# Optimization experiments

Hardware: AMD Instinct MI355X
Metric: run time of the kernel (lower is better)

## Reference

```python
import jax, jax.numpy as jnp
import numpy as np

SQRT3 = float(np.sqrt(3.0))
TWO_PI = float(2.0 * np.pi)


def _safe_sqrt(x):
    return jnp.sqrt(jnp.clip(x, 1e-5))


def _matern(Q):
    # Matern 3/2 on the (already halved) quadratic form, matching torch matern()
    t = SQRT3 * _safe_sqrt(Q)
    return (1.0 + t) * jnp.exp(-t)


def _pairwise_kernel(x1, kp1, x2, kp2, scale):
    """Fused prob_product_quad + prob_product_constant + matern.

    x: [B,N,2] coords; kp: [B,N,3] = (e00, e11, e01) of SPD 2x2 E per point.
    Returns K [B,N,M].
    """
    a1, b1, c1 = kp1[..., 0], kp1[..., 1], kp1[..., 2]  # e00, e11, e01
    a2, b2, c2 = kp2[..., 0], kp2[..., 1], kp2[..., 2]
    det1 = a1 * b1 - c1 * c1  # det2x2(E1) [B,N]
    det2 = a2 * b2 - c2 * c2  # [B,M]
    s00 = a1[:, :, None] + a2[:, None, :]  # E1_00 + E2_00  [B,N,M]
    s11 = b1[:, :, None] + b2[:, None, :]
    s01 = c1[:, :, None] + c2[:, None, :]
    sdet = s00 * s11 - s01 * s01  # det(E1+E2)
    d = x1[:, :, None, :] - x2[:, None, :, :]  # [B,N,M,2]
    d0, d1 = d[..., 0], d[..., 1]
    Q = (s11 * d0 * d0 - 2.0 * s01 * d0 * d1 + s00 * d1 * d1) / sdet * 0.5
    C = 2.0 * (det1 ** 0.25)[:, :, None] * (det2 ** 0.25)[:, None, :] / _safe_sqrt(sdet)
    return _matern(Q) * C * scale


def _diag_kernel(kp, scale):
    # diagonal_prob_product: Q = 0, C = 2*sqrt(det E)/safe_sqrt(det(2E))
    a, b, c = kp[..., 0], kp[..., 1], kp[..., 2]
    det = a * b - c * c
    det2E = 4.0 * det  # det(2E) for 2x2
    C = 2.0 * jnp.sqrt(det) / _safe_sqrt(det2E)
    Q = jnp.zeros_like(C)
    return C * _matern(Q) * scale  # [B,N]


def setup_inputs() -> dict:
    key = jax.random.key(0)
    ks = jax.random.split(key, 8)
    B, N, M = 2, 1024, 16384

    def kparams(k, n):
        u = jax.random.uniform(k, (B, n, 3), dtype=jnp.float32)
        a = 0.5 + u[..., 0]
        b = 0.5 + u[..., 1]
        c = 0.2 * (u[..., 2] - 0.5)  # |c| small -> SPD
        return jnp.stack([a, b, c], axis=-1)

    coords_train = jax.random.uniform(ks[0], (B, N, 2), dtype=jnp.float32) * 512.0 / 64.0
    coords_test = jax.random.uniform(ks[1], (B, M, 2), dtype=jnp.float32) * 512.0 / 64.0
    kernel_params_train = kparams(ks[2], N)
    kernel_params_test = kparams(ks[3], M)
    y_train = jax.random.uniform(ks[4], (B, N, 1), dtype=jnp.float32) * 10.0
    var = 0.01 + 0.1 * jax.random.uniform(ks[5], (B, N), dtype=jnp.float32)
    mean = jnp.zeros((B, 1, 1), dtype=jnp.float32)
    scale_param = jnp.zeros((1,), dtype=jnp.float32)
    return {
        "coords_train": coords_train,
        "kernel_params_train": kernel_params_train,
        "coords_test": coords_test,
        "kernel_params_test": kernel_params_test,
        "y_train": y_train,
        "var": var,
        "mean": mean,
        "scale_param": scale_param,
    }


def reference(coords_train, kernel_params_train, coords_test, kernel_params_test,
              y_train, var, mean, scale_param):
    scale_prior = 1.0
    scale = scale_prior * jnp.exp(scale_param[0])  # CovarianceModule.get_scale
    B, N = coords_train.shape[0], coords_train.shape[1]

    # CovarianceModule / CrossCovarianceModule / DiagonalCovarianceModule
    K_nn = _pairwise_kernel(coords_train, kernel_params_train,
                            coords_train, kernel_params_train, scale)  # [B,N,N]
    K_nm = _pairwise_kernel(coords_train, kernel_params_train,
                            coords_test, kernel_params_test, scale)    # [B,N,M]
    K_mm_diag = _diag_kernel(kernel_params_test, scale)                 # [B,M]

    # GpSparseModule: A = K_nn + diag(var); chol; alpha = A^{-1}(y-mean); NLML
    eye = jnp.eye(N, dtype=K_nn.dtype)
    A = K_nn + var[..., None] * eye
    L = jnp.linalg.cholesky(A)
    y_centered = y_train - mean
    alpha = jax.scipy.linalg.cho_solve((L, True), y_centered)  # [B,N,1]
    data_fit = jnp.sum(y_centered * alpha, axis=1)             # [B,1]
    data_term = 0.5 * jnp.sum(data_fit, axis=1)                # [B]
    complexity_term = jnp.sum(jnp.log(jnp.diagonal(L, axis1=-2, axis2=-1)), axis=1)
    constant_term = 0.5 * N * np.log(TWO_PI)
    nlml = data_term + complexity_term + constant_term

    # GpDenseModule: predictive mean/variance at test points
    pred_mean = mean + jnp.einsum('bnm,bnk->bmk', K_nm, alpha)  # [B,M,1]
    v = jax.scipy.linalg.cho_solve((L, True), K_nm)             # [B,N,M]
    pred_var = (K_mm_diag - jnp.sum(K_nm * v, axis=1))[..., None]  # [B,M,1]
    return pred_mean, pred_var, nlml
```

## Files before the change

### kernel.cpp

```cpp
#include <hip/hip_runtime.h>
#include <math.h>

namespace {
constexpr int kB = 2;
constexpr int kN = 1024;
constexpr int kM = 16384;
constexpr float kSqrt3 = 1.7320508075688772f;

constexpr size_t A_BYTES = (size_t)kB * kN * kN * 4;
constexpr size_t DG_BYTES = (size_t)kB * 8 * 128 * 128 * 4;
constexpr size_t Z_BYTES = (size_t)kB * kN * 4;
constexpr size_t LH_BYTES = (size_t)kB * kN * kN * 2;
constexpr size_t DH_BYTES = (size_t)kB * 8 * 128 * 128 * 2;
constexpr size_t A_OFF = 0;
constexpr size_t DG_OFF = A_OFF + A_BYTES;
constexpr size_t Z_OFF = DG_OFF + DG_BYTES;
constexpr size_t LH_OFF = Z_OFF + Z_BYTES;
constexpr size_t LL_OFF = LH_OFF + LH_BYTES;
constexpr size_t DH_OFF = LL_OFF + LH_BYTES;
constexpr size_t DL_OFF = DH_OFF + DH_BYTES;
constexpr size_t WS_BYTES = DL_OFF + DH_BYTES;
}

typedef __attribute__((ext_vector_type(8))) short short8v;
typedef __attribute__((ext_vector_type(4))) float floatx4;

__device__ __forceinline__ float b16f(unsigned short h) {
  return __uint_as_float(((unsigned)h) << 16);
}
__device__ __forceinline__ void split_bf16(float x, unsigned short& h, unsigned short& l) {
  unsigned u = __float_as_uint(x);
  h = (unsigned short)(u >> 16);
  float rem = x - b16f(h);
  l = (unsigned short)(__float_as_uint(rem) >> 16);
}
__device__ __forceinline__ void pack2(float v0, float v1, unsigned& hw, unsigned& lw) {
  unsigned u0 = __float_as_uint(v0), u1 = __float_as_uint(v1);
  unsigned h0 = u0 & 0xFFFF0000u;
  unsigned h1 = u1 & 0xFFFF0000u;
  hw = (h0 >> 16) | h1;
  float r0 = v0 - __uint_as_float(h0);
  float r1 = v1 - __uint_as_float(h1);
  lw = (__float_as_uint(r0) >> 16) | (__float_as_uint(r1) & 0xFFFF0000u);
}

__device__ __forceinline__ float pair_kernel(
    float x0, float x1, float a1, float b1, float c1,
    float y0, float y1, float a2, float b2, float c2, float scale) {
  float det1 = a1 * b1 - c1 * c1;
  float det2 = a2 * b2 - c2 * c2;
  float s00 = a1 + a2, s11 = b1 + b2, s01 = c1 + c2;
  float sdet = s00 * s11 - s01 * s01;
  float d0 = x0 - y0, d1 = x1 - y1;
  float quad = s11 * d0 * d0 - 2.0f * s01 * d0 * d1 + s00 * d1 * d1;
  float Q = __fdividef(0.5f * quad, sdet);
  float x3 = 3.0f * fmaxf(Q, 1e-5f);
  float t = x3 * rsqrtf(x3);
  float C = 2.0f * sqrtf(sqrtf(det1)) * sqrtf(sqrtf(det2)) * rsqrtf(fmaxf(sdet, 1e-5f));
  return (1.0f + t) * __expf(-t) * C * scale;
}

__global__ __launch_bounds__(256) void build_A(
    const float* __restrict__ xt, const float* __restrict__ pt,
    const float* __restrict__ var, const float* __restrict__ sp,
    float* __restrict__ A) {
  int idx = blockIdx.x * 256 + threadIdx.x;
  int b = idx / (kN * kN);
  int r = (idx / kN) % kN;
  int c = idx % kN;
  float scale = __expf(sp[0]);
  const float* x1 = xt + ((size_t)b * kN + r) * 2;
  const float* p1 = pt + ((size_t)b * kN + r) * 3;
  const float* x2 = xt + ((size_t)b * kN + c) * 2;
  const float* p2 = pt + ((size_t)b * kN + c) * 3;
  float k = pair_kernel(x1[0], x1[1], p1[0], p1[1], p1[2],
                        x2[0], x2[1], p2[0], p2[1], p2[2], scale);
  if (r == c) k += var[b * kN + r];
  A[(size_t)idx] = k;
}

__device__ __forceinline__ void tri_decode(int idx, int& ti, int& tj) {
  float f = sqrtf(8.0f * (float)idx + 1.0f);
  int t0 = (int)((f - 1.0f) * 0.5f);
  while (t0 * (t0 + 1) / 2 > idx) --t0;
  while ((t0 + 1) * (t0 + 2) / 2 <= idx) ++t0;
  ti = t0;
  tj = idx - t0 * (t0 + 1) / 2;
}

__global__ __launch_bounds__(1024, 1) void chol_panel(float* __restrict__ A,
                                                      float* __restrict__ Dg,
                                                      unsigned short* __restrict__ Dh,
                                                      unsigned short* __restrict__ Dl, int p) {
  __shared__ float At[128 * 132];
  __shared__ float Dt[128 * 132];
  __shared__ float Tt[3 * 32 * 33];
  int b = blockIdx.x, t = threadIdx.x;
  float* Ab = A + (size_t)b * kN * kN;
  int r0 = p * 128;
#pragma unroll
  for (int q = 0; q < 4; ++q) {
    int idx = t + 1024 * q;
    int r = idx >> 5, c4 = idx & 31;
    *(float4*)&At[r * 132 + c4 * 4] = *(const float4*)&Ab[(size_t)(r0 + r) * kN + r0 + c4 * 4];
  }
  __syncthreads();
  int wave = t >> 6, lane = t & 63;
  int row0 = lane, row1 = lane + 64;
  for (int kb = 0; kb < 16; ++kb) {
    int K0 = kb * 8;
    int Kp = K0 - 8;
    if (kb > 0) {
      if (wave == 0) {
        int rr = lane >> 3, cc = lane & 7;
        float s = 0.0f;
#pragma unroll
        for (int e = 0; e < 8; ++e)
          s += At[(K0 + rr) * 132 + Kp + e] * At[(K0 + cc) * 132 + Kp + e];
        At[(K0 + rr) * 132 + K0 + cc] -= s;
      } else {
        int n = 120 - 8 * kb;
        int nt = n >> 2;
        int ntt = nt * (nt + 1) / 2;
        int base = K0 + 8;
        for (int idx = t - 64; idx < ntt; idx += 960) {
          int ti, tj;
          tri_decode(idx, ti, tj);
          int i0 = base + ti * 4, j0 = base + tj * 4;
          float Li[4][8], Lj[4][8];
#pragma unroll
          for (int r = 0; r < 4; ++r) {
            *(float4*)&Li[r][0] = *(const float4*)&At[(i0 + r) * 132 + Kp];
            *(float4*)&Li[r][4] = *(const float4*)&At[(i0 + r) * 132 + Kp + 4];
            *(float4*)&Lj[r][0] = *(const float4*)&At[(j0 + r) * 132 + Kp];
            *(float4*)&Lj[r][4] = *(const float4*)&At[(j0 + r) * 132 + Kp + 4];
          }
#pragma unroll
          for (int r = 0; r < 4; ++r) {
            float4 cv = *(const float4*)&At[(i0 + r) * 132 + j0];
            float cc4[4] = {cv.x, cv.y, cv.z, cv.w};
#pragma unroll
            for (int c = 0; c < 4; ++c) {
              float s = 0.0f;
#pragma unroll
              for (int e = 0; e < 8; ++e) s += Li[r][e] * Lj[c][e];
              cc4[c] -= s;
            }
            float4 ov = {cc4[0], cc4[1], cc4[2], cc4[3]};
            *(float4*)&At[(i0 + r) * 132 + j0] = ov;
          }
        }
      }
    }
    __syncthreads();
    if (wave == 0) {
      float rA0[8], rA1[8];
      *(float4*)&rA0[0] = *(const float4*)&At[row0 * 132 + K0];
      *(float4*)&rA0[4] = *(const float4*)&At[row0 * 132 + K0 + 4];
      *(float4*)&rA1[0] = *(const float4*)&At[row1 * 132 + K0];
      *(float4*)&rA1[4] = *(const float4*)&At[row1 * 132 + K0 + 4];
      if (kb > 0) {
        float pA0[8], pA1[8];
        *(float4*)&pA0[0] = *(const float4*)&At[row0 * 132 + Kp];
        *(float4*)&pA0[4] = *(const float4*)&At[row0 * 132 + Kp + 4];
        *(float4*)&pA1[0] = *(const float4*)&At[row1 * 132 + Kp];
        *(float4*)&pA1[4] = *(const float4*)&At[row1 * 132 + Kp + 4];
#pragma unroll
        for (int j = 0; j < 8; ++j) {
          float s0 = 0.0f, s1 = 0.0f;
#pragma unroll
          for (int e = 0; e < 8; ++e) {
            float pj = At[(K0 + j) * 132 + Kp + e];
            s0 += pA0[e] * pj;
            s1 += pA1[e] * pj;
          }
          rA0[j] -= s0;
          rA1[j] -= s1;
        }
      }
      float L11[8][8], idg[8];
#pragma unroll
      for (int r = 0; r < 8; ++r) {
        *(float4*)&L11[r][0] = *(const float4*)&At[(K0 + r) * 132 + K0];
        *(float4*)&L11[r][4] = *(const float4*)&At[(K0 + r) * 132 + K0 + 4];
      }
#pragma unroll
      for (int c = 0; c < 8; ++c) {
        float d = sqrtf(L11[c][c]);
        float iv = 1.0f / d;
        idg[c] = iv;
        L11[c][c] = d;
#pragma unroll
        for (int i = c + 1; i < 8; ++i) L11[i][c] *= iv;
#pragma unroll
        for (int j = c + 1; j < 8; ++j)
#pragma unroll
          for (int i = j; i < 8; ++i) L11[i][j] -= L11[i][c] * L11[j][c];
      }
      if (row0 >= K0 + 8) {
#pragma unroll
        for (int c = 0; c < 8; ++c) {
          float s = rA0[c];
#pragma unroll
          for (int j = 0; j < c; ++j) s -= rA0[j] * L11[c][j];
          rA0[c] = s * idg[c];
        }
      } else if (row0 >= K0) {
#pragma unroll
        for (int rr = 0; rr < 8; ++rr)
          if (row0 - K0 == rr) {
#pragma unroll
            for (int e = 0; e < 8; ++e) rA0[e] = (e <= rr) ? L11[rr][e] : 0.0f;
          }
      }
      if (row1 >= K0 + 8) {
#pragma unroll
        for (int c = 0; c < 8; ++c) {
          float s = rA1[c];
#pragma unroll
          for (int j = 0; j < c; ++j) s -= rA1[j] * L11[c][j];
          rA1[c] = s * idg[c];
        }
      } else if (row1 >= K0) {
#pragma unroll
        for (int rr = 0; rr < 8; ++rr)
          if (row1 - K0 == rr) {
#pragma unroll
            for (int e = 0; e < 8; ++e) rA1[e] = (e <= rr) ? L11[rr][e] : 0.0f;
          }
      }
      if (row0 >= K0) {
        float4 v0 = {rA0[0], rA0[1], rA0[2], rA0[3]};
        float4 v1 = {rA0[4], rA0[5], rA0[6], rA0[7]};
        *(float4*)&At[row0 * 132 + K0] = v0;
        *(float4*)&At[row0 * 132 + K0 + 4] = v1;
      }
      if (row1 >= K0) {
        float4 v0 = {rA1[0], rA1[1], rA1[2], rA1[3]};
        float4 v1 = {rA1[4], rA1[5], rA1[6], rA1[7]};
        *(float4*)&At[row1 * 132 + K0] = v0;
        *(float4*)&At[row1 * 132 + K0 + 4] = v1;
      }
    }
    __syncthreads();
  }
  if (t < 128) {
    int q = t >> 5, c = t & 31, bse = q * 32;
    float x[32];
#pragma unroll
    for (int r = 0; r < 32; ++r) {
      float s = (r == c) ? 1.0f : 0.0f;
#pragma unroll
      for (int j = 0; j < 32; ++j)
        if (j < r) s -= At[(bse + r) * 132 + bse + j] * x[j];
      x[r] = (r < c) ? 0.0f : s / At[(bse + r) * 132 + bse + r];
    }
#pragma unroll
    for (int r = 0; r < 32; ++r) Dt[(bse + r) * 132 + bse + c] = x[r];
  }
  __syncthreads();
  {
    int r = t >> 5, cl = t & 31;
    for (int s = 1; s <= 3; ++s) {
      for (int blk = 0; blk < 4 - s; ++blk) {
        int J = blk, I = J + s;
        float sum = 0.0f;
        for (int K = J; K < I; ++K)
          for (int j = 0; j < 32; ++j)
            sum += At[(I * 32 + r) * 132 + K * 32 + j] * Dt[(K * 32 + j) * 132 + J * 32 + cl];
        Tt[blk * (32 * 33) + r * 33 + cl] = sum;
      }
      __syncthreads();
      for (int blk = 0; blk < 4 - s; ++blk) {
        int J = blk, I = J + s;
        float sum = 0.0f;
        for (int j = 0; j < 32; ++j)
          sum += Dt[(I * 32 + r) * 132 + I * 32 + j] * Tt[blk * (32 * 33) + j * 33 + cl];
        Dt[(I * 32 + r) * 132 + J * 32 + cl] = -sum;
      }
      __syncthreads();
    }
  }
#pragma unroll
  for (int q = 0; q < 4; ++q) {
    int jj = t + 1024 * q;
    int r = jj >> 5, ch = jj & 31;
    int c0 = ch * 4;
    float4 v = *(const float4*)&At[r * 132 + c0];
    v.x = (c0 + 0 <= r) ? v.x : 0.0f;
    v.y = (c0 + 1 <= r) ? v.y : 0.0f;
    v.z = (c0 + 2 <= r) ? v.z : 0.0f;
    v.w = (c0 + 3 <= r) ? v.w : 0.0f;
    *(float4*)&Ab[(size_t)(r0 + r) * kN + r0 + c0] = v;
  }
  float* Db = Dg + (size_t)(b * 8 + p) * 16384;
  unsigned short* Dhb = Dh + (size_t)(b * 8 + p) * 16384;
  unsigned short* Dlb = Dl + (size_t)(b * 8 + p) * 16384;
#pragma unroll
  for (int q = 0; q < 4; ++q) {
    int jj = t + 1024 * q;
    int r = jj >> 5, ch = jj & 31;
    int c0 = ch * 4;
    float4 v = *(const float4*)&Dt[r * 132 + c0];
    v.x = (c0 + 0 <= r) ? v.x : 0.0f;
    v.y = (c0 + 1 <= r) ? v.y : 0.0f;
    v.z = (c0 + 2 <= r) ? v.z : 0.0f;
    v.w = (c0 + 3 <= r) ? v.w : 0.0f;
    *(float4*)&Db[r * 128 + c0] = v;
    float vv[4] = {v.x, v.y, v.z, v.w};
    unsigned short hs[4], ls[4];
#pragma unroll
    for (int e = 0; e < 4; ++e) split_bf16(vv[e], hs[e], ls[e]);
    *(ushort4*)&Dhb[r * 128 + c0] = make_ushort4(hs[0], hs[1], hs[2], hs[3]);
    *(ushort4*)&Dlb[r * 128 + c0] = make_ushort4(ls[0], ls[1], ls[2], ls[3]);
  }
}

__global__ __launch_bounds__(256) void chol_trsm(float* __restrict__ A,
                                                 const float* __restrict__ Dg,
                                                 unsigned short* __restrict__ Lh,
                                                 unsigned short* __restrict__ Ll, int p) {
  __shared__ float At[128 * 129];
  __shared__ float Dt[128 * 129];
  int b = blockIdx.y, rb = blockIdx.x;
  int rs = (p + 1 + rb) * 128;
  float* Ab = A + (size_t)b * kN * kN;
  const float* Db = Dg + (size_t)(b * 8 + p) * 16384;
  int t = threadIdx.x;
  for (int q = 0; q < 64; ++q) {
    int li = t + 256 * q;
    int r = li >> 7, cc = li & 127;
    At[r * 129 + cc] = Ab[(size_t)(rs + r) * kN + p * 128 + cc];
    Dt[r * 129 + cc] = Db[r * 128 + cc];
  }
  __syncthreads();
  int tx = t & 15, ty = t >> 4;
  float acc[8][8] = {};
  for (int j = 0; j < 128; ++j) {
    float a[8], d[8];
#pragma unroll
    for (int q = 0; q < 8; ++q) a[q] = At[(ty * 8 + q) * 129 + j];
#pragma unroll
    for (int q = 0; q < 8; ++q) d[q] = Dt[(tx * 8 + q) * 129 + j];
#pragma unroll
    for (int qr = 0; qr < 8; ++qr)
#pragma unroll
      for (int qc = 0; qc < 8; ++qc) acc[qr][qc] = fmaf(a[qr], d[qc], acc[qr][qc]);
  }
#pragma unroll
  for (int qr = 0; qr < 8; ++qr)
#pragma unroll
    for (int qc = 0; qc < 8; ++qc) {
      float v = acc[qr][qc];
      Ab[(size_t)(rs + ty * 8 + qr) * kN + p * 128 + tx * 8 + qc] = v;
      size_t lo = ((size_t)b * kN + rs + ty * 8 + qr) * kN + p * 128 + tx * 8 + qc;
      unsigned short h, l;
      split_bf16(-v, h, l);
      Lh[lo] = h;
      Ll[lo] = l;
    }
}

__global__ __launch_bounds__(256) void chol_syrk(float* __restrict__ A, int p) {
  __shared__ float L1t[128 * 129];
  __shared__ float L2t[128 * 129];
  int b = blockIdx.y;
  int pid = blockIdx.x;
  int bi = 0;
  while ((bi + 1) * (bi + 2) / 2 <= pid) ++bi;
  int bj = pid - bi * (bi + 1) / 2;
  int rs1 = (p + 1 + bi) * 128, rs2 = (p + 1 + bj) * 128;
  float* Ab = A + (size_t)b * kN * kN;
  int t = threadIdx.x;
  for (int q = 0; q < 64; ++q) {
    int li = t + 256 * q;
    int r = li >> 7, cc = li & 127;
    L1t[r * 129 + cc] = Ab[(size_t)(rs1 + r) * kN + p * 128 + cc];
    L2t[r * 129 + cc] = Ab[(size_t)(rs2 + r) * kN + p * 128 + cc];
  }
  __syncthreads();
  int tx = t & 15, ty = t >> 4;
  float acc[8][8] = {};
  for (int j = 0; j < 128; ++j) {
    float a[8], d[8];
#pragma unroll
    for (int q = 0; q < 8; ++q) a[q] = L1t[(ty * 8 + q) * 129 + j];
#pragma unroll
    for (int q = 0; q < 8; ++q) d[q] = L2t[(tx * 8 + q) * 129 + j];
#pragma unroll
    for (int qr = 0; qr < 8; ++qr)
#pragma unroll
      for (int qc = 0; qc < 8; ++qc) acc[qr][qc] = fmaf(a[qr], d[qc], acc[qr][qc]);
  }
#pragma unroll
  for (int qr = 0; qr < 8; ++qr)
#pragma unroll
    for (int qc = 0; qc < 8; ++qc) {
      size_t o = (size_t)(rs1 + ty * 8 + qr) * kN + rs2 + tx * 8 + qc;
      Ab[o] -= acc[qr][qc];
    }
}

__global__ __launch_bounds__(128) void solve_small(
    const float* __restrict__ A, const float* __restrict__ Dg,
    const float* __restrict__ y, const float* __restrict__ meanp,
    float* __restrict__ zbuf, float* __restrict__ out) {
  __shared__ __align__(16) float zs[1024];
  __shared__ float ts[128];
  __shared__ float red[128];
  int b = blockIdx.x, t = threadIdx.x;
  const float* Ab = A + (size_t)b * kN * kN;
  float mv = meanp[b];
  for (int q = t; q < 1024; q += 128) zs[q] = y[b * kN + q] - mv;
  __syncthreads();
  for (int i = 0; i < 8; ++i) {
    float acc = zs[i * 128 + t];
    const float* Lrow = Ab + (size_t)(i * 128 + t) * kN;
    for (int kk = 0; kk < i * 128; kk += 4) {
      float4 lv = *(const float4*)&Lrow[kk];
      float4 zv = *(const float4*)&zs[kk];
      acc -= lv.x * zv.x + lv.y * zv.y + lv.z * zv.z + lv.w * zv.w;
    }
    ts[t] = acc;
    __syncthreads();
    const float* Db = Dg + (size_t)(b * 8 + i) * 16384 + t * 128;
    float zv = 0.0f;
    for (int c = 0; c <= t; ++c) zv += Db[c] * ts[c];
    zs[i * 128 + t] = zv;
    __syncthreads();
  }
  float df = 0.0f, ld = 0.0f;
  for (int q = t; q < 1024; q += 128) {
    df += zs[q] * zs[q];
    ld += logf(Ab[(size_t)q * kN + q]);
  }
  red[t] = df;
  __syncthreads();
  for (int s = 64; s > 0; s >>= 1) {
    if (t < s) red[t] += red[t + s];
    __syncthreads();
  }
  float dfs = red[0];
  __syncthreads();
  red[t] = ld;
  __syncthreads();
  for (int s = 64; s > 0; s >>= 1) {
    if (t < s) red[t] += red[t + s];
    __syncthreads();
  }
  if (t == 0)
    out[2 * kB * kM + b] = 0.5f * dfs + red[0] + 0.5f * 1024.0f * logf(6.283185307179586f);
  for (int q = t; q < 1024; q += 128) zbuf[b * kN + q] = zs[q];
}

__global__ __launch_bounds__(256, 2) void fused_mfma(
    const unsigned short* __restrict__ Lh, const unsigned short* __restrict__ Ll,
    const unsigned short* __restrict__ Dh, const unsigned short* __restrict__ Dl,
    const float* __restrict__ xt, const float* __restrict__ pt,
    const float* __restrict__ xs, const float* __restrict__ ps,
    const float* __restrict__ sp, const float* __restrict__ meanp,
    const float* __restrict__ zbuf, float* __restrict__ out) {
  __shared__ unsigned short Th[32 * 144];
  __shared__ unsigned short Tl[32 * 144];
  __shared__ float trp[128 * 6];
  __shared__ float tp[32 * 6];
  __shared__ float zs[128];
  __shared__ float red[32 * 16 * 2];
  int mt = blockIdx.x, b = blockIdx.y;
  int t = threadIdx.x;
  int lane = t & 63, wave = t >> 6;
  int lrow = lane & 15, kgrp = lane >> 4;
  float scale = __expf(sp[0]);
  if (t < 32) {
    int mg = mt * 32 + t;
    float x0 = xs[((size_t)b * kM + mg) * 2 + 0];
    float x1 = xs[((size_t)b * kM + mg) * 2 + 1];
    float a = ps[((size_t)b * kM + mg) * 3 + 0];
    float bb = ps[((size_t)b * kM + mg) * 3 + 1];
    float c = ps[((size_t)b * kM + mg) * 3 + 2];
    float det2 = a * bb - c * c;
    tp[t * 6 + 0] = x0; tp[t * 6 + 1] = x1; tp[t * 6 + 2] = a;
    tp[t * 6 + 3] = bb; tp[t * 6 + 4] = c; tp[t * 6 + 5] = sqrtf(sqrtf(det2));
  }
  floatx4 W[8][2][2];
#pragma unroll
  for (int i = 0; i < 8; ++i)
#pragma unroll
    for (int rf = 0; rf < 2; ++rf)
#pragma unroll
      for (int cf = 0; cf < 2; ++cf) W[i][rf][cf] = (floatx4){0.f, 0.f, 0.f, 0.f};
  float pma[2] = {0.f, 0.f}, s2a[2] = {0.f, 0.f};

#pragma unroll
  for (int k = 0; k < 8; ++k) {
    __syncthreads();
    if (t < 128) {
      size_t n = (size_t)b * kN + k * 128 + t;
      float x0 = xt[n * 2 + 0];
      float x1 = xt[n * 2 + 1];
      float a = pt[n * 3 + 0];
      float bb = pt[n * 3 + 1];
      float c = pt[n * 3 + 2];
      float det1 = a * bb - c * c;
      trp[t * 6 + 0] = x0; trp[t * 6 + 1] = x1; trp[t * 6 + 2] = a;
      trp[t * 6 + 3] = bb; trp[t * 6 + 4] = c;
      trp[t * 6 + 5] = 2.0f * scale * sqrtf(sqrtf(det1));
      zs[t] = zbuf[n];
    }
    __syncthreads();
#pragma unroll
    for (int rf = 0; rf < 2; ++rf) {
      int n0 = wave * 32 + rf * 16 + kgrp * 4;
      float nx0[4], nx1[4], na[4], nb[4], nc[4], nc1[4];
#pragma unroll
      for (int r = 0; r < 4; ++r) {
        int n = n0 + r;
        nx0[r] = trp[n * 6 + 0]; nx1[r] = trp[n * 6 + 1]; na[r] = trp[n * 6 + 2];
        nb[r] = trp[n * 6 + 3]; nc[r] = trp[n * 6 + 4]; nc1[r] = trp[n * 6 + 5];
      }
#pragma unroll
      for (int cf = 0; cf < 2; ++cf) {
        int m = cf * 16 + lrow;
        float mx0 = tp[m * 6 + 0], mx1 = tp[m * 6 + 1], ma = tp[m * 6 + 2];
        float mb = tp[m * 6 + 3], mc = tp[m * 6 + 4], mq = tp[m * 6 + 5];
        float Tv[4];
#pragma unroll
        for (int r = 0; r < 4; ++r) {
          float s00 = na[r] + ma, s11 = nb[r] + mb, s01 = nc[r] + mc;
          float sdet = s00 * s11 - s01 * s01;
          float d0 = nx0[r] - mx0, d1 = nx1[r] - mx1;
          float quad = s11 * d0 * d0 - 2.0f * s01 * d0 * d1 + s00 * d1 * d1;
          float Q = __fdividef(0.5f * quad, sdet);
          float x3 = 3.0f * fmaxf(Q, 1e-5f);
          float tt = x3 * rsqrtf(x3);
          float Kv = (1.0f + tt) * __expf(-tt) * nc1[r] * (mq * rsqrtf(fmaxf(sdet, 1e-5f)));
          Tv[r] = Kv + W[k][rf][cf][r];
        }
        unsigned hw[2], lw[2];
        pack2(Tv[0], Tv[1], hw[0], lw[0]);
        pack2(Tv[2], Tv[3], hw[1], lw[1]);
        int off = m * 144 + n0;
        *(uint2*)&Th[off] = make_uint2(hw[0], hw[1]);
        *(uint2*)&Tl[off] = make_uint2(lw[0], lw[1]);
      }
    }
    __syncthreads();
    floatx4 wk[2][2];
#pragma unroll
    for (int rf = 0; rf < 2; ++rf)
#pragma unroll
      for (int cf = 0; cf < 2; ++cf) wk[rf][cf] = (floatx4){0.f, 0.f, 0.f, 0.f};
    {
      const unsigned short* Dhb = Dh + (size_t)(b * 8 + k) * 16384;
      const unsigned short* Dlb = Dl + (size_t)(b * 8 + k) * 16384;
#pragma unroll
      for (int ks = 0; ks < 4; ++ks) {
        short8v bh[2], bl[2];
#pragma unroll
        for (int cf = 0; cf < 2; ++cf) {
          int boff = (cf * 16 + lrow) * 144 + ks * 32 + kgrp * 8;
          bh[cf] = *(const short8v*)&Th[boff];
          bl[cf] = *(const short8v*)&Tl[boff];
        }
        short8v ah[2], al[2];
#pragma unroll
        for (int rf = 0; rf < 2; ++rf) {
          size_t aoff = (size_t)(wave * 32 + rf * 16 + lrow) * 128 + ks * 32 + kgrp * 8;
          ah[rf] = *(const short8v*)&Dhb[aoff];
          al[rf] = *(const short8v*)&Dlb[aoff];
        }
#pragma unroll
        for (int rf = 0; rf < 2; ++rf)
#pragma unroll
          for (int cf = 0; cf < 2; ++cf) {
            wk[rf][cf] = __builtin_amdgcn_mfma_f32_16x16x32_bf16(ah[rf], bh[cf], wk[rf][cf], 0, 0, 0);
            wk[rf][cf] = __builtin_amdgcn_mfma_f32_16x16x32_bf16(ah[rf], bl[cf], wk[rf][cf], 0, 0, 0);
            wk[rf][cf] = __builtin_amdgcn_mfma_f32_16x16x32_bf16(al[rf], bh[cf], wk[rf][cf], 0, 0, 0);
          }
      }
    }
    __syncthreads();
#pragma unroll
    for (int rf = 0; rf < 2; ++rf) {
      int n0 = wave * 32 + rf * 16 + kgrp * 4;
#pragma unroll
      for (int cf = 0; cf < 2; ++cf) {
        int m = cf * 16 + lrow;
        float wv[4];
#pragma unroll
        for (int r = 0; r < 4; ++r) {
          wv[r] = wk[rf][cf][r];
          pma[cf] = fmaf(wv[r], zs[n0 + r], pma[cf]);
          s2a[cf] = fmaf(wv[r], wv[r], s2a[cf]);
        }
        unsigned hw[2], lw[2];
        pack2(wv[0], wv[1], hw[0], lw[0]);
        pack2(wv[2], wv[3], hw[1], lw[1]);
        int off = m * 144 + n0;
        *(uint2*)&Th[off] = make_uint2(hw[0], hw[1]);
        *(uint2*)&Tl[off] = make_uint2(lw[0], lw[1]);
      }
    }
    __syncthreads();
    __builtin_amdgcn_s_setprio(1);
#pragma unroll
    for (int ks = 0; ks < 4; ++ks) {
      short8v bh[2], bl[2];
#pragma unroll
      for (int cf = 0; cf < 2; ++cf) {
        int boff = (cf * 16 + lrow) * 144 + ks * 32 + kgrp * 8;
        bh[cf] = *(const short8v*)&Th[boff];
        bl[cf] = *(const short8v*)&Tl[boff];
      }
#pragma unroll
      for (int i = k + 1; i < 8; ++i) {
        short8v ah[2], al[2];
#pragma unroll
        for (int rf = 0; rf < 2; ++rf) {
          size_t ro = (size_t)b * kN + i * 128 + wave * 32 + rf * 16 + lrow;
          size_t aoff = ro * kN + k * 128 + ks * 32 + kgrp * 8;
          ah[rf] = *(const short8v*)&Lh[aoff];
          al[rf] = *(const short8v*)&Ll[aoff];
        }
#pragma unroll
        for (int rf = 0; rf < 2; ++rf)
#pragma unroll
          for (int cf = 0; cf < 2; ++cf) {
            W[i][rf][cf] = __builtin_amdgcn_mfma_f32_16x16x32_bf16(ah[rf], bh[cf], W[i][rf][cf], 0, 0, 0);
            W[i][rf][cf] = __builtin_amdgcn_mfma_f32_16x16x32_bf16(ah[rf], bl[cf], W[i][rf][cf], 0, 0, 0);
            W[i][rf][cf] = __builtin_amdgcn_mfma_f32_16x16x32_bf16(al[rf], bh[cf], W[i][rf][cf], 0, 0, 0);
          }
      }
    }
    __builtin_amdgcn_s_setprio(0);
  }
  __syncthreads();
#pragma unroll
  for (int cf = 0; cf < 2; ++cf) {
    int m = cf * 16 + lrow;
    red[m * 16 + wave * 4 + kgrp] = pma[cf];
    red[512 + m * 16 + wave * 4 + kgrp] = s2a[cf];
  }
  __syncthreads();
  if (t < 32) {
    float pm = 0.f, s2 = 0.f;
#pragma unroll
    for (int j = 0; j < 16; ++j) {
      pm += red[t * 16 + j];
      s2 += red[512 + t * 16 + j];
    }
    int mg = mt * 32 + t;
    float a = tp[t * 6 + 2], bb = tp[t * 6 + 3], c = tp[t * 6 + 4];
    float det = a * bb - c * c;
    float C = 2.0f * sqrtf(det) * rsqrtf(fmaxf(4.0f * det, 1e-5f));
    float t0 = kSqrt3 * sqrtf(1e-5f);
    float mat = (1.0f + t0) * __expf(-t0);
    float kd = C * mat * scale;
    out[b * kM + mg] = meanp[b] + pm;
    out[kB * kM + b * kM + mg] = kd - s2;
  }
}

extern "C" void kernel_launch(void* const* d_in, const int* in_sizes, int n_in,
                              void* d_out, int out_size, void* d_ws, size_t ws_size,
                              hipStream_t stream) {
  const float* xt = (const float*)d_in[0];
  const float* pt = (const float*)d_in[1];
  const float* xs = (const float*)d_in[2];
  const float* ps = (const float*)d_in[3];
  const float* y = (const float*)d_in[4];
  const float* var = (const float*)d_in[5];
  const float* meanp = (const float*)d_in[6];
  const float* sp = (const float*)d_in[7];
  float* out = (float*)d_out;
  char* ws = (char*)d_ws;
  if (ws_size < WS_BYTES) return;

  float* A = (float*)(ws + A_OFF);
  float* Dg = (float*)(ws + DG_OFF);
  float* zbuf = (float*)(ws + Z_OFF);
  unsigned short* Lh = (unsigned short*)(ws + LH_OFF);
  unsigned short* Ll = (unsigned short*)(ws + LL_OFF);
  unsigned short* Dh = (unsigned short*)(ws + DH_OFF);
  unsigned short* Dl = (unsigned short*)(ws + DL_OFF);

  build_A<<<(kB * kN * kN) / 256, 256, 0, stream>>>(xt, pt, var, sp, A);
  for (int p = 0; p < 8; ++p) {
    chol_panel<<<kB, 1024, 0, stream>>>(A, Dg, Dh, Dl, p);
    if (p < 7) {
      int nt = 7 - p;
      chol_trsm<<<dim3(nt, kB), 256, 0, stream>>>(A, Dg, Lh, Ll, p);
      chol_syrk<<<dim3(nt * (nt + 1) / 2, kB), 256, 0, stream>>>(A, p);
    }
  }
  solve_small<<<kB, 128, 0, stream>>>(A, Dg, y, meanp, zbuf, out);
  fused_mfma<<<dim3(kM / 32, kB), 256, 0, stream>>>(Lh, Ll, Dh, Dl, xt, pt, xs, ps,
                                                    sp, meanp, zbuf, out);
}
```

Measured before the change: 1.281 ms.

## Parallelize small triangular solve across 1024 threads and force-unroll fused k-loop

The forward solve kernel moves from 128 to 1024 threads per batch. It stages L blocks and the diagonal-inverse blocks through shared memory with coalesced float4 loads, and splits each row's dot products across 8 thread groups with a shared-memory partial reduction. This removes the long serial per-thread strided global reads of the old single-block solve. Separately, the fused MFMA kernel's k loop is expanded by a macro so that k is a compile-time constant, which keeps the W[k] register array statically indexed and the inner i-loop bounds fixed. The macro expansion adds code size and register pressure, and the solve adds many more block barriers.

```diff
diff --git a/kernel.cpp b/kernel.cpp
--- a/kernel.cpp
+++ b/kernel.cpp
@@ -401,56 +401,90 @@
     }
 }
 
-__global__ __launch_bounds__(128) void solve_small(
+__global__ __launch_bounds__(1024) void solve_small(
     const float* __restrict__ A, const float* __restrict__ Dg,
     const float* __restrict__ y, const float* __restrict__ meanp,
     float* __restrict__ zbuf, float* __restrict__ out) {
+  __shared__ float Ls[128 * 132];
   __shared__ __align__(16) float zs[1024];
   __shared__ float ts[128];
-  __shared__ float red[128];
+  __shared__ float part[128 * 9];
+  __shared__ float red[1024];
   int b = blockIdx.x, t = threadIdx.x;
+  int row = t & 127, g = t >> 7;
   const float* Ab = A + (size_t)b * kN * kN;
   float mv = meanp[b];
-  for (int q = t; q < 1024; q += 128) zs[q] = y[b * kN + q] - mv;
+  zs[t] = y[b * kN + t] - mv;
   __syncthreads();
   for (int i = 0; i < 8; ++i) {
-    float acc = zs[i * 128 + t];
-    const float* Lrow = Ab + (size_t)(i * 128 + t) * kN;
-    for (int kk = 0; kk < i * 128; kk += 4) {
-      float4 lv = *(const float4*)&Lrow[kk];
-      float4 zv = *(const float4*)&zs[kk];
-      acc -= lv.x * zv.x + lv.y * zv.y + lv.z * zv.z + lv.w * zv.w;
-    }
-    ts[t] = acc;
+    float ps = 0.0f;
+    for (int k = 0; k < i; ++k) {
+#pragma unroll
+      for (int q = 0; q < 4; ++q) {
+        int li = t + 1024 * q;
+        int r = li >> 5, c4 = li & 31;
+        *(float4*)&Ls[r * 132 + c4 * 4] =
+            *(const float4*)&Ab[(size_t)(i * 128 + r) * kN + k * 128 + c4 * 4];
+      }
+      __syncthreads();
+      const float* Lr = &Ls[row * 132 + g * 16];
+      const float* zk = &zs[k * 128 + g * 16];
+#pragma unroll
+      for (int c = 0; c < 16; c += 4) {
+        float4 lv = *(const float4*)&Lr[c];
+        float4 zv = *(const float4*)&zk[c];
+        ps += lv.x * zv.x + lv.y * zv.y + lv.z * zv.z + lv.w * zv.w;
+      }
+      __syncthreads();
+    }
+    part[row * 9 + g] = ps;
+    {
+      const float* Db = Dg + (size_t)(b * 8 + i) * 16384;
+#pragma unroll
+      for (int q = 0; q < 4; ++q) {
+        int li = t + 1024 * q;
+        int r = li >> 5, c4 = li & 31;
+        *(float4*)&Ls[r * 132 + c4 * 4] = *(const float4*)&Db[r * 128 + c4 * 4];
+      }
+    }
     __syncthreads();
-    const float* Db = Dg + (size_t)(b * 8 + i) * 16384 + t * 128;
-    float zv = 0.0f;
-    for (int c = 0; c <= t; ++c) zv += Db[c] * ts[c];
-    zs[i * 128 + t] = zv;
+    if (g == 0) {
+      float acc = zs[i * 128 + row];
+#pragma unroll
+      for (int gg = 0; gg < 8; ++gg) acc -= part[row * 9 + gg];
+      ts[row] = acc;
+    }
     __syncthreads();
-  }
-  float df = 0.0f, ld = 0.0f;
-  for (int q = t; q < 1024; q += 128) {
-    df += zs[q] * zs[q];
-    ld += logf(Ab[(size_t)q * kN + q]);
-  }
-  red[t] = df;
-  __syncthreads();
-  for (int s = 64; s > 0; s >>= 1) {
+    float s = 0.0f;
+    int c0 = g * 16, c1 = min(c0 + 16, row + 1);
+    for (int c = c0; c < c1; ++c) s += Ls[row * 132 + c] * ts[c];
+    part[row * 9 + g] = s;
+    __syncthreads();
+    if (g == 0) {
+      float zv = 0.0f;
+#pragma unroll
+      for (int gg = 0; gg < 8; ++gg) zv += part[row * 9 + gg];
+      zs[i * 128 + row] = zv;
+    }
+    __syncthreads();
+  }
+  red[t] = zs[t] * zs[t];
+  __syncthreads();
+  for (int s = 512; s > 0; s >>= 1) {
     if (t < s) red[t] += red[t + s];
     __syncthreads();
   }
   float dfs = red[0];
   __syncthreads();
-  red[t] = ld;
-  __syncthreads();
-  for (int s = 64; s > 0; s >>= 1) {
+  red[t] = logf(Ab[(size_t)t * kN + t]);
+  __syncthreads();
+  for (int s = 512; s > 0; s >>= 1) {
     if (t < s) red[t] += red[t + s];
     __syncthreads();
   }
   if (t == 0)
     out[2 * kB * kM + b] = 0.5f * dfs + red[0] + 0.5f * 1024.0f * logf(6.283185307179586f);
-  for (int q = t; q < 1024; q += 128) zbuf[b * kN + q] = zs[q];
+  zbuf[b * kN + t] = zs[t];
 }
 
 __global__ __launch_bounds__(256, 2) void fused_mfma(
@@ -491,149 +525,161 @@
       for (int cf = 0; cf < 2; ++cf) W[i][rf][cf] = (floatx4){0.f, 0.f, 0.f, 0.f};
   float pma[2] = {0.f, 0.f}, s2a[2] = {0.f, 0.f};
 
-#pragma unroll
-  for (int k = 0; k < 8; ++k) {
-    __syncthreads();
-    if (t < 128) {
-      size_t n = (size_t)b * kN + k * 128 + t;
-      float x0 = xt[n * 2 + 0];
-      float x1 = xt[n * 2 + 1];
-      float a = pt[n * 3 + 0];
-      float bb = pt[n * 3 + 1];
-      float c = pt[n * 3 + 2];
-      float det1 = a * bb - c * c;
-      trp[t * 6 + 0] = x0; trp[t * 6 + 1] = x1; trp[t * 6 + 2] = a;
-      trp[t * 6 + 3] = bb; trp[t * 6 + 4] = c;
-      trp[t * 6 + 5] = 2.0f * scale * sqrtf(sqrtf(det1));
-      zs[t] = zbuf[n];
-    }
-    __syncthreads();
-#pragma unroll
-    for (int rf = 0; rf < 2; ++rf) {
-      int n0 = wave * 32 + rf * 16 + kgrp * 4;
-      float nx0[4], nx1[4], na[4], nb[4], nc[4], nc1[4];
-#pragma unroll
-      for (int r = 0; r < 4; ++r) {
-        int n = n0 + r;
-        nx0[r] = trp[n * 6 + 0]; nx1[r] = trp[n * 6 + 1]; na[r] = trp[n * 6 + 2];
-        nb[r] = trp[n * 6 + 3]; nc[r] = trp[n * 6 + 4]; nc1[r] = trp[n * 6 + 5];
-      }
-#pragma unroll
-      for (int cf = 0; cf < 2; ++cf) {
-        int m = cf * 16 + lrow;
-        float mx0 = tp[m * 6 + 0], mx1 = tp[m * 6 + 1], ma = tp[m * 6 + 2];
-        float mb = tp[m * 6 + 3], mc = tp[m * 6 + 4], mq = tp[m * 6 + 5];
-        float Tv[4];
-#pragma unroll
-        for (int r = 0; r < 4; ++r) {
-          float s00 = na[r] + ma, s11 = nb[r] + mb, s01 = nc[r] + mc;
-          float sdet = s00 * s11 - s01 * s01;
-          float d0 = nx0[r] - mx0, d1 = nx1[r] - mx1;
-          float quad = s11 * d0 * d0 - 2.0f * s01 * d0 * d1 + s00 * d1 * d1;
-          float Q = __fdividef(0.5f * quad, sdet);
-          float x3 = 3.0f * fmaxf(Q, 1e-5f);
-          float tt = x3 * rsqrtf(x3);
-          float Kv = (1.0f + tt) * __expf(-tt) * nc1[r] * (mq * rsqrtf(fmaxf(sdet, 1e-5f)));
-          Tv[r] = Kv + W[k][rf][cf][r];
-        }
-        unsigned hw[2], lw[2];
-        pack2(Tv[0], Tv[1], hw[0], lw[0]);
-        pack2(Tv[2], Tv[3], hw[1], lw[1]);
-        int off = m * 144 + n0;
-        *(uint2*)&Th[off] = make_uint2(hw[0], hw[1]);
-        *(uint2*)&Tl[off] = make_uint2(lw[0], lw[1]);
-      }
-    }
-    __syncthreads();
-    floatx4 wk[2][2];
-#pragma unroll
-    for (int rf = 0; rf < 2; ++rf)
-#pragma unroll
-      for (int cf = 0; cf < 2; ++cf) wk[rf][cf] = (floatx4){0.f, 0.f, 0.f, 0.f};
-    {
-      const unsigned short* Dhb = Dh + (size_t)(b * 8 + k) * 16384;
-      const unsigned short* Dlb = Dl + (size_t)(b * 8 + k) * 16384;
-#pragma unroll
-      for (int ks = 0; ks < 4; ++ks) {
-        short8v bh[2], bl[2];
-#pragma unroll
-        for (int cf = 0; cf < 2; ++cf) {
-          int boff = (cf * 16 + lrow) * 144 + ks * 32 + kgrp * 8;
-          bh[cf] = *(const short8v*)&Th[boff];
-          bl[cf] = *(const short8v*)&Tl[boff];
-        }
-        short8v ah[2], al[2];
-#pragma unroll
-        for (int rf = 0; rf < 2; ++rf) {
-          size_t aoff = (size_t)(wave * 32 + rf * 16 + lrow) * 128 + ks * 32 + kgrp * 8;
-          ah[rf] = *(const short8v*)&Dhb[aoff];
-          al[rf] = *(const short8v*)&Dlb[aoff];
-        }
-#pragma unroll
-        for (int rf = 0; rf < 2; ++rf)
-#pragma unroll
-          for (int cf = 0; cf < 2; ++cf) {
-            wk[rf][cf] = __builtin_amdgcn_mfma_f32_16x16x32_bf16(ah[rf], bh[cf], wk[rf][cf], 0, 0, 0);
-            wk[rf][cf] = __builtin_amdgcn_mfma_f32_16x16x32_bf16(ah[rf], bl[cf], wk[rf][cf], 0, 0, 0);
-            wk[rf][cf] = __builtin_amdgcn_mfma_f32_16x16x32_bf16(al[rf], bh[cf], wk[rf][cf], 0, 0, 0);
-          }
-      }
-    }
-    __syncthreads();
-#pragma unroll
-    for (int rf = 0; rf < 2; ++rf) {
-      int n0 = wave * 32 + rf * 16 + kgrp * 4;
-#pragma unroll
-      for (int cf = 0; cf < 2; ++cf) {
-        int m = cf * 16 + lrow;
-        float wv[4];
-#pragma unroll
-        for (int r = 0; r < 4; ++r) {
-          wv[r] = wk[rf][cf][r];
-          pma[cf] = fmaf(wv[r], zs[n0 + r], pma[cf]);
-          s2a[cf] = fmaf(wv[r], wv[r], s2a[cf]);
-        }
-        unsigned hw[2], lw[2];
-        pack2(wv[0], wv[1], hw[0], lw[0]);
-        pack2(wv[2], wv[3], hw[1], lw[1]);
-        int off = m * 144 + n0;
-        *(uint2*)&Th[off] = make_uint2(hw[0], hw[1]);
-        *(uint2*)&Tl[off] = make_uint2(lw[0], lw[1]);
-      }
-    }
-    __syncthreads();
-    __builtin_amdgcn_s_setprio(1);
-#pragma unroll
-    for (int ks = 0; ks < 4; ++ks) {
-      short8v bh[2], bl[2];
-#pragma unroll
-      for (int cf = 0; cf < 2; ++cf) {
-        int boff = (cf * 16 + lrow) * 144 + ks * 32 + kgrp * 8;
-        bh[cf] = *(const short8v*)&Th[boff];
-        bl[cf] = *(const short8v*)&Tl[boff];
-      }
-#pragma unroll
-      for (int i = k + 1; i < 8; ++i) {
-        short8v ah[2], al[2];
-#pragma unroll
-        for (int rf = 0; rf < 2; ++rf) {
-          size_t ro = (size_t)b * kN + i * 128 + wave * 32 + rf * 16 + lrow;
-          size_t aoff = ro * kN + k * 128 + ks * 32 + kgrp * 8;
-          ah[rf] = *(const short8v*)&Lh[aoff];
-          al[rf] = *(const short8v*)&Ll[aoff];
-        }
-#pragma unroll
-        for (int rf = 0; rf < 2; ++rf)
-#pragma unroll
-          for (int cf = 0; cf < 2; ++cf) {
-            W[i][rf][cf] = __builtin_amdgcn_mfma_f32_16x16x32_bf16(ah[rf], bh[cf], W[i][rf][cf], 0, 0, 0);
-            W[i][rf][cf] = __builtin_amdgcn_mfma_f32_16x16x32_bf16(ah[rf], bl[cf], W[i][rf][cf], 0, 0, 0);
-            W[i][rf][cf] = __builtin_amdgcn_mfma_f32_16x16x32_bf16(al[rf], bh[cf], W[i][rf][cf], 0, 0, 0);
-          }
-      }
-    }
-    __builtin_amdgcn_s_setprio(0);
-  }
+#define FUSED_K_STEP(KC)                                                                   \
+  {                                                                                        \
+    constexpr int k = (KC);                                                                \
+    __syncthreads();                                                                       \
+    if (t < 128) {                                                                         \
+      size_t n = (size_t)b * kN + k * 128 + t;                                             \
+      float x0 = xt[n * 2 + 0];                                                            \
+      float x1 = xt[n * 2 + 1];                                                            \
+      float a = pt[n * 3 + 0];                                                             \
+      float bb = pt[n * 3 + 1];                                                            \
+      float c = pt[n * 3 + 2];                                                             \
+      float det1 = a * bb - c * c;                                                         \
+      trp[t * 6 + 0] = x0; trp[t * 6 + 1] = x1; trp[t * 6 + 2] = a;                        \
+      trp[t * 6 + 3] = bb; trp[t * 6 + 4] = c;                                             \
+      trp[t * 6 + 5] = 2.0f * scale * sqrtf(sqrtf(det1));                                  \
+      zs[t] = zbuf[n];                                                                     \
+    }                                                                                      \
+    __syncthreads();                                                                       \
+    _Pragma("unroll")                                                                      \
+    for (int rf = 0; rf < 2; ++rf) {                                                       \
+      int n0 = wave * 32 + rf * 16 + kgrp * 4;                                             \
+      float nx0[4], nx1[4], na[4], nb[4], nc[4], nc1[4];                                   \
+      _Pragma("unroll")                                                                    \
+      for (int r = 0; r < 4; ++r) {                                                        \
+        int n = n0 + r;                                                                    \
+        nx0[r] = trp[n * 6 + 0]; nx1[r] = trp[n * 6 + 1]; na[r] = trp[n * 6 + 2];          \
+        nb[r] = trp[n * 6 + 3]; nc[r] = trp[n * 6 + 4]; nc1[r] = trp[n * 6 + 5];           \
+      }                                                                                    \
+      _Pragma("unroll")                                                                    \
+      for (int cf = 0; cf < 2; ++cf) {                                                     \
+        int m = cf * 16 + lrow;                                                            \
+        float mx0 = tp[m * 6 + 0], mx1 = tp[m * 6 + 1], ma = tp[m * 6 + 2];                \
+        float mb = tp[m * 6 + 3], mc = tp[m * 6 + 4], mq = tp[m * 6 + 5];                  \
+        float Tv[4];                                                                       \
+        _Pragma("unroll")                                                                  \
+        for (int r = 0; r < 4; ++r) {                                                      \
+          float s00 = na[r] + ma, s11 = nb[r] + mb, s01 = nc[r] + mc;                      \
+          float sdet = s00 * s11 - s01 * s01;                                              \
+          float d0 = nx0[r] - mx0, d1 = nx1[r] - mx1;                                      \
+          float quad = s11 * d0 * d0 - 2.0f * s01 * d0 * d1 + s00 * d1 * d1;               \
+          float Q = __fdividef(0.5f * quad, sdet);                                         \
+          float x3 = 3.0f * fmaxf(Q, 1e-5f);                                               \
+          float tt = x3 * rsqrtf(x3);                                                      \
+          float Kv = (1.0f + tt) * __expf(-tt) * nc1[r] * (mq * rsqrtf(fmaxf(sdet, 1e-5f))); \
+          Tv[r] = Kv + W[k][rf][cf][r];                                                    \
+        }                                                                                  \
+        unsigned hw[2], lw[2];                                                             \
+        pack2(Tv[0], Tv[1], hw[0], lw[0]);                                                 \
+        pack2(Tv[2], Tv[3], hw[1], lw[1]);                                                 \
+        int off = m * 144 + n0;                                                            \
+        *(uint2*)&Th[off] = make_uint2(hw[0], hw[1]);                                      \
+        *(uint2*)&Tl[off] = make_uint2(lw[0], lw[1]);                                      \
+      }                                                                                    \
+    }                                                                                      \
+    __syncthreads();                                                                       \
+    floatx4 wk[2][2];                                                                      \
+    _Pragma("unroll")                                                                      \
+    for (int rf = 0; rf < 2; ++rf)                                                         \
+      _Pragma("unroll")                                                                    \
+      for (int cf = 0; cf < 2; ++cf) wk[rf][cf] = (floatx4){0.f, 0.f, 0.f, 0.f};           \
+    {                                                                                      \
+      const unsigned short* Dhb = Dh + (size_t)(b * 8 + k) * 16384;                        \
+      const unsigned short* Dlb = Dl + (size_t)(b * 8 + k) * 16384;                        \
+      _Pragma("unroll")                                                                    \
+      for (int ks = 0; ks < 4; ++ks) {                                                     \
+        short8v bh[2], bl[2];                                                              \
+        _Pragma("unroll")                                                                  \
+        for (int cf = 0; cf < 2; ++cf) {                                                   \
+          int boff = (cf * 16 + lrow) * 144 + ks * 32 + kgrp * 8;                          \
+          bh[cf] = *(const short8v*)&Th[boff];                                             \
+          bl[cf] = *(const short8v*)&Tl[boff];                                             \
+        }                                                                                  \
+        short8v ah[2], al[2];                                                              \
+        _Pragma("unroll")                                                                  \
+        for (int rf = 0; rf < 2; ++rf) {                                                   \
+          size_t aoff = (size_t)(wave * 32 + rf * 16 + lrow) * 128 + ks * 32 + kgrp * 8;   \
+          ah[rf] = *(const short8v*)&Dhb[aoff];                                            \
+          al[rf] = *(const short8v*)&Dlb[aoff];                                            \
+        }                                                                                  \
+        _Pragma("unroll")                                                                  \
+        for (int rf = 0; rf < 2; ++rf)                                                     \
+          _Pragma("unroll")                                                                \
+          for (int cf = 0; cf < 2; ++cf) {                                                 \
+            wk[rf][cf] = __builtin_amdgcn_mfma_f32_16x16x32_bf16(ah[rf], bh[cf], wk[rf][cf], 0, 0, 0); \
+            wk[rf][cf] = __builtin_amdgcn_mfma_f32_16x16x32_bf16(ah[rf], bl[cf], wk[rf][cf], 0, 0, 0); \
+            wk[rf][cf] = __builtin_amdgcn_mfma_f32_16x16x32_bf16(al[rf], bh[cf], wk[rf][cf], 0, 0, 0); \
+          }                                                                                \
+      }                                                                                    \
+    }                                                                                      \
+    __syncthreads();                                                                       \
+    _Pragma("unroll")                                                                      \
+    for (int rf = 0; rf < 2; ++rf) {                                                       \
+      int n0 = wave * 32 + rf * 16 + kgrp * 4;                                             \
+      _Pragma("unroll")                                                                    \
+      for (int cf = 0; cf < 2; ++cf) {                                                     \
+        int m = cf * 16 + lrow;                                                            \
+        float wv[4];                                                                       \
+        _Pragma("unroll")                                                                  \
+        for (int r = 0; r < 4; ++r) {                                                      \
+          wv[r] = wk[rf][cf][r];                                                           \
+          pma[cf] = fmaf(wv[r], zs[n0 + r], pma[cf]);                                      \
+          s2a[cf] = fmaf(wv[r], wv[r], s2a[cf]);                                           \
+        }                                                                                  \
+        unsigned hw[2], lw[2];                                                             \
+        pack2(wv[0], wv[1], hw[0], lw[0]);                                                 \
+        pack2(wv[2], wv[3], hw[1], lw[1]);                                                 \
+        int off = m * 144 + n0;                                                            \
+        *(uint2*)&Th[off] = make_uint2(hw[0], hw[1]);                                      \
+        *(uint2*)&Tl[off] = make_uint2(lw[0], lw[1]);                                      \
+      }                                                                                    \
+    }                                                                                      \
+    __syncthreads();                                                                       \
+    __builtin_amdgcn_s_setprio(1);                                                         \
+    _Pragma("unroll")                                                                      \
+    for (int ks = 0; ks < 4; ++ks) {                                                       \
+      short8v bh[2], bl[2];                                                                \
+      _Pragma("unroll")                                                                    \
+      for (int cf = 0; cf < 2; ++cf) {                                                     \
+        int boff = (cf * 16 + lrow) * 144 + ks * 32 + kgrp * 8;                            \
+        bh[cf] = *(const short8v*)&Th[boff];                                               \
+        bl[cf] = *(const short8v*)&Tl[boff];                                               \
+      }                                                                                    \
+      _Pragma("unroll")                                                                    \
+      for (int i = k + 1; i < 8; ++i) {                                                    \
+        short8v ah[2], al[2];                                                              \
+        _Pragma("unroll")                                                                  \
+        for (int rf = 0; rf < 2; ++rf) {                                                   \
+          size_t ro = (size_t)b * kN + i * 128 + wave * 32 + rf * 16 + lrow;               \
+          size_t aoff = ro * kN + k * 128 + ks * 32 + kgrp * 8;                            \
+          ah[rf] = *(const short8v*)&Lh[aoff];                                             \
+          al[rf] = *(const short8v*)&Ll[aoff];                                             \
+        }                                                                                  \
+        _Pragma("unroll")                                                                  \
+        for (int rf = 0; rf < 2; ++rf)                                                     \
+          _Pragma("unroll")                                                                \
+          for (int cf = 0; cf < 2; ++cf) {                                                 \
+            W[i][rf][cf] = __builtin_amdgcn_mfma_f32_16x16x32_bf16(ah[rf], bh[cf], W[i][rf][cf], 0, 0, 0); \
+            W[i][rf][cf] = __builtin_amdgcn_mfma_f32_16x16x32_bf16(ah[rf], bl[cf], W[i][rf][cf], 0, 0, 0); \
+            W[i][rf][cf] = __builtin_amdgcn_mfma_f32_16x16x32_bf16(al[rf], bh[cf], W[i][rf][cf], 0, 0, 0); \
+          }                                                                                \
+      }                                                                                    \
+    }                                                                                      \
+    __builtin_amdgcn_s_setprio(0);                                                         \
+  }
+
+  FUSED_K_STEP(0)
+  FUSED_K_STEP(1)
+  FUSED_K_STEP(2)
+  FUSED_K_STEP(3)
+  FUSED_K_STEP(4)
+  FUSED_K_STEP(5)
+  FUSED_K_STEP(6)
+  FUSED_K_STEP(7)
+#undef FUSED_K_STEP
+
   __syncthreads();
 #pragma unroll
   for (int cf = 0; cf < 2; ++cf) {
@@ -693,7 +739,7 @@
       chol_syrk<<<dim3(nt * (nt + 1) / 2, kB), 256, 0, stream>>>(A, p);
     }
   }
-  solve_small<<<kB, 128, 0, stream>>>(A, Dg, y, meanp, zbuf, out);
+  solve_small<<<kB, 1024, 0, stream>>>(A, Dg, y, meanp, zbuf, out);
   fused_mfma<<<dim3(kM / 32, kB), 256, 0, stream>>>(Lh, Ll, Dh, Dl, xt, pt, xs, ps,
                                                     sp, meanp, zbuf, out);
 }
```

Result: faster. 1.232 ms (-3.8%).
